# Kernel optimization log

Measured on AMD Instinct MI355X. Metric: run time of the kernel, lower is better.

The kernel has to match this reference:

```python
import jax, jax.numpy as jnp
import numpy as np

N_NODES = 100000
N_EDGES = 1600000
MAX_RADIUS = 3.0
NUM_BASIS = 3
SQRT2 = 2.0 ** 0.5
# e3nn soft_one_hot_linspace 'smooth_finite' prefactor
C_SMOOTH = 1.14136 * float(np.exp(2.0))


def _sus(x):
    # smooth unit step: exp(-1/x) for x>0 else 0 (NaN-safe for grad)
    safe = jnp.where(x > 0.0, x, 1.0)
    return jnp.where(x > 0.0, jnp.exp(-1.0 / safe), 0.0)


def radial_embed(d):
    # soft_one_hot_linspace(d, 0, max_radius, 3, basis='smooth_finite', cutoff=True) * sqrt(num_basis)
    values = jnp.linspace(0.0, MAX_RADIUS, NUM_BASIS + 2)[1:-1]  # [3]
    step = MAX_RADIUS / (NUM_BASIS + 1)
    diff = (d[:, None] - values) / step  # [E,3]
    y = C_SMOOTH * _sus(diff + 1.0) * _sus(1.0 - diff)
    return y * (NUM_BASIS ** 0.5)


def fcnet(x, w1, w2):
    # e3nn FullyConnectedNet([3,16,numel], relu): normalized weights, normalize2mom(relu)=sqrt(2)*relu
    h = SQRT2 * jax.nn.relu(x @ (w1 / w1.shape[0] ** 0.5))
    return h @ (w2 / w2.shape[0] ** 0.5)


def reference(pos, feat, edge_src, edge_dst, fc1_w1, fc1_w2, core_w1, core_w2, fc3_w1, fc3_w2, conv_w, conv_b):
    n = pos.shape[0]
    z = edge_src.shape[0] / n  # average num neighbors
    edge_vec = pos[edge_dst] - pos[edge_src]
    d = jnp.sqrt(jnp.sum(edge_vec * edge_vec, axis=1))  # edges are self-loop-free -> d > 0
    emb = radial_embed(d)  # [E,3]

    # NOTE on e3nn math: with input/mid/output parities all even and sh = 0e+1o+2e,
    # the only parity-allowed paths producing nonzero output are the 0e (scalar) paths,
    # which contract against Y_0 = 1 ('component' normalization). The 4x1e block of the
    # mid irreps is identically zero (no parity-allowed path ever populates it), so the
    # math below (scalar block only, with e3nn path weights) is exactly equivalent.
    def conv(x, w1, w2, mul_in, mul_out, path_w):
        # per-edge weights from radial MLP; keep the 0e->0e instruction block
        w = fcnet(emb, w1, w2)[:, : mul_in * mul_out].reshape(-1, mul_in, mul_out)
        msg = path_w * jnp.einsum('euw,eu->ew', w, x[edge_src])
        return jax.ops.segment_sum(msg, edge_dst, num_segments=n) / z ** 0.5

    x = conv(feat, fc1_w1, fc1_w2, 3, 4, (1.0 / 3.0) ** 0.5)  # tp1: fan_in 3*1 -> pw=1/sqrt(3)
    for i in range(3):
        x = conv(x, core_w1[i], core_w2[i], 4, 4, 0.5)  # tp2 0e path: pw=sqrt(1/4)
    x = conv(x, fc3_w1, fc3_w2, 4, 16, 0.5)  # tp3: pw=sqrt(1/4)
    # Conv1d(16, 2, 1) == pointwise linear
    return x @ conv_w.T + conv_b


def setup_inputs():
    key = jax.random.key(0)
    ks = jax.random.split(key, 12)
    pos = jax.random.uniform(ks[0], (N_NODES, 3), dtype=jnp.float32)  # unit box -> all edge lengths < max_radius
    feat = jax.random.normal(ks[1], (N_NODES, 3), dtype=jnp.float32)
    edge_src = jax.random.randint(ks[2], (N_EDGES,), 0, N_NODES, dtype=jnp.int32)
    off = jax.random.randint(ks[3], (N_EDGES,), 1, N_NODES, dtype=jnp.int32)
    edge_dst = ((edge_src + off) % N_NODES).astype(jnp.int32)  # radius_graph has no self-loops
    return {
        'pos': pos,
        'feat': feat,
        'edge_src': edge_src,
        'edge_dst': edge_dst,
        'fc1_w1': jax.random.normal(ks[4], (3, 16), jnp.float32),
        'fc1_w2': jax.random.normal(ks[5], (16, 12), jnp.float32),
        'core_w1': jax.random.normal(ks[6], (3, 3, 16), jnp.float32),
        'core_w2': jax.random.normal(ks[7], (3, 16, 48), jnp.float32),
        'fc3_w1': jax.random.normal(ks[8], (3, 16), jnp.float32),
        'fc3_w2': jax.random.normal(ks[9], (16, 64), jnp.float32),
        'conv_w': jax.random.normal(ks[10], (2, 16), jnp.float32) * 0.25,
        'conv_b': jax.random.normal(ks[11], (2,), jnp.float32) * 0.1,
    }
```

## Files before the change

### kernel.cpp

```cpp
#include <hip/hip_runtime.h>


#define BCAP 4608
#define NBMAX 400

__device__ __forceinline__ float sus_f(float x) {
    return x > 0.0f ? __expf(-1.0f / x) : 0.0f;
}

__device__ __forceinline__ float uload(const float* p) {
    return __uint_as_float(__builtin_amdgcn_readfirstlane(__float_as_uint(*p)));
}

__global__ __launch_bounds__(1024) void k_bin(
    const int* __restrict__ src, const int* __restrict__ dst,
    int* __restrict__ gcur, int* __restrict__ ptmp,
    const float* __restrict__ fc3w2, const float* __restrict__ cw,
    float* __restrict__ gbuf,
    int nedges, int nb)
{
    __shared__ int cnt[NBMAX];
    __shared__ int gb[NBMAX];
    __shared__ int lscan[NBMAX];
    __shared__ int tot;
    __shared__ unsigned short map[8192];
    __shared__ int lpk[8192];

    int t = threadIdx.x;
    if (t < NBMAX) cnt[t] = 0;
    __syncthreads();

    int base = blockIdx.x * 8192 + t * 8;
    int pk[8]; int bk[8]; short r[8];
    int ss[8], dd[8];
    if (base + 7 < nedges) {
        int4 s0 = *(const int4*)&src[base];
        int4 s1 = *(const int4*)&src[base + 4];
        int4 d0 = *(const int4*)&dst[base];
        int4 d1 = *(const int4*)&dst[base + 4];
        ss[0]=s0.x; ss[1]=s0.y; ss[2]=s0.z; ss[3]=s0.w;
        ss[4]=s1.x; ss[5]=s1.y; ss[6]=s1.z; ss[7]=s1.w;
        dd[0]=d0.x; dd[1]=d0.y; dd[2]=d0.z; dd[3]=d0.w;
        dd[4]=d1.x; dd[5]=d1.y; dd[6]=d1.z; dd[7]=d1.w;
        #pragma unroll
        for (int i = 0; i < 8; ++i) {
            int b = dd[i] >> 8;
            bk[i] = b;
            pk[i] = (ss[i] << 8) | (dd[i] & 255);
            r[i] = (short)atomicAdd(&cnt[b], 1);
        }
    } else {
        #pragma unroll
        for (int i = 0; i < 8; ++i) {
            int e = base + i;
            if (e < nedges) {
                int s = src[e], tt = dst[e];
                int b = tt >> 8;
                bk[i] = b;
                pk[i] = (s << 8) | (tt & 255);
                r[i] = (short)atomicAdd(&cnt[b], 1);
            } else bk[i] = -1;
        }
    }
    __syncthreads();

    if (t < 64) {
        int bs = t * 7;
        int c[7]; int s = 0;
        #pragma unroll
        for (int i = 0; i < 7; ++i) {
            int idx = bs + i;
            c[i] = (idx < NBMAX) ? cnt[idx] : 0;
            s += c[i];
        }
        int x = s;
        #pragma unroll
        for (int off = 1; off < 64; off <<= 1) {
            int y = __shfl_up(x, off);
            if (t >= off) x += y;
        }
        int run = x - s;
        #pragma unroll
        for (int i = 0; i < 7; ++i) {
            int idx = bs + i;
            if (idx < NBMAX) lscan[idx] = run;
            run += c[i];
        }
        if (t == 63) tot = run;
    }
    if (t < NBMAX && t < nb) {
        int c = cnt[t];
        gb[t] = c > 0 ? atomicAdd(&gcur[t], c) : 0;
    }
    __syncthreads();

    #pragma unroll
    for (int i = 0; i < 8; ++i) {
        if (bk[i] >= 0) lpk[lscan[bk[i]] + (int)r[i]] = pk[i];
    }
    if (t < NBMAX && t < nb) {
        int beg = lscan[t], end = beg + cnt[t];
        for (int j = beg; j < end; ++j) map[j] = (unsigned short)t;
    }
    __syncthreads();

    for (int j = t; j < tot; j += 1024) {
        int b = map[j];
        int p = gb[b] + (j - lscan[b]);
        if (p < BCAP)
            ptmp[b * BCAP + p] = lpk[j];
    }

    if (blockIdx.x == 0 && t < 128) {
        int idx = t;
        int k = idx >> 3, u = (idx >> 1) & 3, c = idx & 1;
        float s = 0.0f;
        #pragma unroll
        for (int w = 0; w < 16; ++w)
            s = fmaf(fc3w2[k * 64 + u * 16 + w], cw[c * 16 + w], s);
        gbuf[idx] = s;
    }
}

__global__ __launch_bounds__(1024) void k_build(
    const int* __restrict__ gcur, const int* __restrict__ ptmp,
    const float* __restrict__ pos,
    float4* __restrict__ ebuf, int2* __restrict__ offs2,
    int n, int nb)
{
    int b = blockIdx.x;
    int cnt = gcur[b]; if (cnt > BCAP) cnt = BCAP;
    int t = threadIdx.x;

    __shared__ int stage[BCAP];
    __shared__ int perm[BCAP];
    __shared__ int deg[256];
    __shared__ int loffs[256];
    __shared__ int cur[256];

    const int* tin = ptmp + b * BCAP;
    for (int j = t; j < cnt; j += 1024) stage[j] = tin[j];
    if (t < 256) deg[t] = 0;
    __syncthreads();

    for (int j = t; j < cnt; j += 1024)
        atomicAdd(&deg[stage[j] & 255], 1);
    __syncthreads();

    if (t < 64) {
        int d0 = deg[4 * t + 0], d1 = deg[4 * t + 1];
        int d2 = deg[4 * t + 2], d3 = deg[4 * t + 3];
        int s = d0 + d1 + d2 + d3;
        int x = s;
        #pragma unroll
        for (int off = 1; off < 64; off <<= 1) {
            int y = __shfl_up(x, off);
            if (t >= off) x += y;
        }
        int ex = x - s;
        int e0 = ex, e1 = ex + d0, e2 = e1 + d1, e3 = e2 + d2;
        loffs[4 * t + 0] = e0; cur[4 * t + 0] = e0;
        loffs[4 * t + 1] = e1; cur[4 * t + 1] = e1;
        loffs[4 * t + 2] = e2; cur[4 * t + 2] = e2;
        loffs[4 * t + 3] = e3; cur[4 * t + 3] = e3;
    }
    __syncthreads();

    int nid0 = b << 8;
    {
        int nn = n - nid0; if (nn > 256) nn = 256;
        if (t < nn) {
            int st = b * BCAP + loffs[t];
            offs2[nid0 + t] = make_int2(st, st + deg[t]);
        }
    }

    for (int j = t; j < cnt; j += 1024) {
        int pkd = stage[j];
        perm[atomicAdd(&cur[pkd & 255], 1)] = pkd;
    }
    __syncthreads();

    const float C = 1.14136f * 7.3890560989306495f;
    for (int j = t; j < cnt; j += 1024) {
        int pkd = perm[j];
        int s = pkd >> 8;
        int tt = nid0 | (pkd & 255);
        float dx = pos[3 * tt + 0] - pos[3 * s + 0];
        float dy = pos[3 * tt + 1] - pos[3 * s + 1];
        float dz = pos[3 * tt + 2] - pos[3 * s + 2];
        float d = sqrtf(dx * dx + dy * dy + dz * dz);
        float e0, e1, e2;
        { float f = (d - 0.75f) * (1.0f / 0.75f);
          e0 = C * sus_f(f + 1.0f) * sus_f(1.0f - f); }
        { float f = (d - 1.50f) * (1.0f / 0.75f);
          e1 = C * sus_f(f + 1.0f) * sus_f(1.0f - f); }
        { float f = (d - 2.25f) * (1.0f / 0.75f);
          e2 = C * sus_f(f + 1.0f) * sus_f(1.0f - f); }
        ebuf[(size_t)b * BCAP + j] = make_float4(__int_as_float(s), e0, e1, e2);
    }
}


__global__ __launch_bounds__(256) void k_node_l1(
    const float* __restrict__ feat, const float4* __restrict__ edata,
    const int2* __restrict__ offs2,
    const float* __restrict__ w1, const float* __restrict__ w2,
    float* __restrict__ xout, int n)
{
    __shared__ float lw[16 * 20];
    if (threadIdx.x < 192) {
        int k = threadIdx.x / 12, r = threadIdx.x % 12;
        lw[k * 20 + r] = w2[k * 12 + r];
    }
    __syncthreads();

    int g = blockIdx.x * 256 + threadIdx.x;
    int nd = g >> 2;
    if (nd >= n) return;
    int t = g & 3;

    float w1r[3][16];
    #pragma unroll
    for (int j = 0; j < 3; ++j)
        #pragma unroll
        for (int k = 0; k < 16; ++k) w1r[j][k] = uload(&w1[j * 16 + k]);

    float O[16][3];
    #pragma unroll
    for (int k = 0; k < 16; ++k)
        #pragma unroll
        for (int u = 0; u < 3; ++u) O[k][u] = 0.0f;

    int2 se = offs2[nd];
    int e = se.x + t;
    if (e < se.y) {
        float4 ed = edata[e];
        int e1 = e + 4;
        float4 edn = edata[e1 < se.y ? e1 : e];
        int s = __float_as_int(ed.x);
        float f0 = feat[3 * s + 0], f1 = feat[3 * s + 1], f2 = feat[3 * s + 2];
        while (true) {
            bool more = e1 < se.y;
            int e2 = e1 + 4;
            float4 ed2 = edata[(more && e2 < se.y) ? e2 : e];
            int sn = __float_as_int(edn.x);
            int sp = more ? sn : s;
            float f0n = feat[3 * sp + 0];
            float f1n = feat[3 * sp + 1];
            float f2n = feat[3 * sp + 2];
            #pragma unroll
            for (int k = 0; k < 16; ++k) {
                float a = fmaf(ed.y, w1r[0][k], fmaf(ed.z, w1r[1][k], ed.w * w1r[2][k]));
                float h = a > 0.0f ? a : 0.0f;
                O[k][0] = fmaf(h, f0, O[k][0]);
                O[k][1] = fmaf(h, f1, O[k][1]);
                O[k][2] = fmaf(h, f2, O[k][2]);
            }
            if (!more) break;
            ed = edn; edn = ed2;
            f0 = f0n; f1 = f1n; f2 = f2n;
            e1 = e2;
        }
    }

    float p0 = 0.f, p1 = 0.f, p2 = 0.f, p3 = 0.f;
    #pragma unroll
    for (int k = 0; k < 16; ++k)
        #pragma unroll
        for (int u = 0; u < 3; ++u) {
            const float4 q = *(const float4*)&lw[k * 20 + u * 4];
            float o = O[k][u];
            p0 = fmaf(o, q.x, p0); p1 = fmaf(o, q.y, p1);
            p2 = fmaf(o, q.z, p2); p3 = fmaf(o, q.w, p3);
        }
    p0 += __shfl_xor(p0, 1); p1 += __shfl_xor(p1, 1);
    p2 += __shfl_xor(p2, 1); p3 += __shfl_xor(p3, 1);
    p0 += __shfl_xor(p0, 2); p1 += __shfl_xor(p1, 2);
    p2 += __shfl_xor(p2, 2); p3 += __shfl_xor(p3, 2);
    if (t == 0) {
        const float S = 0.051031036307982884f;
        float4 o; o.x = p0 * S; o.y = p1 * S; o.z = p2 * S; o.w = p3 * S;
        ((float4*)xout)[nd] = o;
    }
}

__global__ __launch_bounds__(256) void k_node_core(
    const float4* __restrict__ xin, const float4* __restrict__ edata,
    const int2* __restrict__ offs2,
    const float* __restrict__ w1, const float* __restrict__ w2,
    float* __restrict__ xout, int n)
{
    __shared__ float lw[16 * 20];
    {
        int idx = threadIdx.x;
        int k = idx >> 4, r = idx & 15;
        lw[k * 20 + r] = w2[k * 48 + r];
    }
    __syncthreads();

    int g = blockIdx.x * 256 + threadIdx.x;
    int nd = g >> 2;
    if (nd >= n) return;
    int t = g & 3;

    float w1r[3][16];
    #pragma unroll
    for (int j = 0; j < 3; ++j)
        #pragma unroll
        for (int k = 0; k < 16; ++k) w1r[j][k] = uload(&w1[j * 16 + k]);

    float O[16][4];
    #pragma unroll
    for (int k = 0; k < 16; ++k)
        #pragma unroll
        for (int u = 0; u < 4; ++u) O[k][u] = 0.0f;

    int2 se = offs2[nd];
    int e = se.x + t;
    if (e < se.y) {
        float4 ed = edata[e];
        int e1 = e + 4;
        float4 edn = edata[e1 < se.y ? e1 : e];
        float4 x = xin[__float_as_int(ed.x)];
        while (true) {
            bool more = e1 < se.y;
            int e2 = e1 + 4;
            float4 ed2 = edata[(more && e2 < se.y) ? e2 : e];
            int sn = __float_as_int(edn.x);
            float4 xn = xin[more ? sn : __float_as_int(ed.x)];
            #pragma unroll
            for (int k = 0; k < 16; ++k) {
                float a = fmaf(ed.y, w1r[0][k], fmaf(ed.z, w1r[1][k], ed.w * w1r[2][k]));
                float h = a > 0.0f ? a : 0.0f;
                O[k][0] = fmaf(h, x.x, O[k][0]);
                O[k][1] = fmaf(h, x.y, O[k][1]);
                O[k][2] = fmaf(h, x.z, O[k][2]);
                O[k][3] = fmaf(h, x.w, O[k][3]);
            }
            if (!more) break;
            ed = edn; edn = ed2; x = xn; e1 = e2;
        }
    }

    float p0 = 0.f, p1 = 0.f, p2 = 0.f, p3 = 0.f;
    #pragma unroll
    for (int k = 0; k < 16; ++k)
        #pragma unroll
        for (int u = 0; u < 4; ++u) {
            const float4 q = *(const float4*)&lw[k * 20 + u * 4];
            float o = O[k][u];
            p0 = fmaf(o, q.x, p0); p1 = fmaf(o, q.y, p1);
            p2 = fmaf(o, q.z, p2); p3 = fmaf(o, q.w, p3);
        }
    p0 += __shfl_xor(p0, 1); p1 += __shfl_xor(p1, 1);
    p2 += __shfl_xor(p2, 1); p3 += __shfl_xor(p3, 1);
    p0 += __shfl_xor(p0, 2); p1 += __shfl_xor(p1, 2);
    p2 += __shfl_xor(p2, 2); p3 += __shfl_xor(p3, 2);
    if (t == 0) {
        const float S = 0.04419417382415922f;
        float4 o; o.x = p0 * S; o.y = p1 * S; o.z = p2 * S; o.w = p3 * S;
        ((float4*)xout)[nd] = o;
    }
}

__global__ __launch_bounds__(256) void k_node_fc3_final(
    const float4* __restrict__ xin, const float4* __restrict__ edata,
    const int2* __restrict__ offs2,
    const float* __restrict__ w1, const float* __restrict__ gbuf,
    const float* __restrict__ cb,
    float* __restrict__ out, int n)
{
    __shared__ float lg[128];
    if (threadIdx.x < 128) lg[threadIdx.x] = gbuf[threadIdx.x];
    __syncthreads();

    int g = blockIdx.x * 256 + threadIdx.x;
    int nd = g >> 2;
    if (nd >= n) return;
    int t = g & 3;

    float w1r[3][16];
    #pragma unroll
    for (int j = 0; j < 3; ++j)
        #pragma unroll
        for (int k = 0; k < 16; ++k) w1r[j][k] = uload(&w1[j * 16 + k]);

    float O[16][4];
    #pragma unroll
    for (int k = 0; k < 16; ++k)
        #pragma unroll
        for (int u = 0; u < 4; ++u) O[k][u] = 0.0f;

    int2 se = offs2[nd];
    int e = se.x + t;
    if (e < se.y) {
        float4 ed = edata[e];
        int e1 = e + 4;
        float4 edn = edata[e1 < se.y ? e1 : e];
        float4 x = xin[__float_as_int(ed.x)];
        while (true) {
            bool more = e1 < se.y;
            int e2 = e1 + 4;
            float4 ed2 = edata[(more && e2 < se.y) ? e2 : e];
            int sn = __float_as_int(edn.x);
            float4 xn = xin[more ? sn : __float_as_int(ed.x)];
            #pragma unroll
            for (int k = 0; k < 16; ++k) {
                float a = fmaf(ed.y, w1r[0][k], fmaf(ed.z, w1r[1][k], ed.w * w1r[2][k]));
                float h = a > 0.0f ? a : 0.0f;
                O[k][0] = fmaf(h, x.x, O[k][0]);
                O[k][1] = fmaf(h, x.y, O[k][1]);
                O[k][2] = fmaf(h, x.z, O[k][2]);
                O[k][3] = fmaf(h, x.w, O[k][3]);
            }
            if (!more) break;
            ed = edn; edn = ed2; x = xn; e1 = e2;
        }
    }

    float a0 = 0.f, a1 = 0.f;
    #pragma unroll
    for (int k = 0; k < 16; ++k)
        #pragma unroll
        for (int u = 0; u < 4; ++u) {
            float o = O[k][u];
            const float2 q = *(const float2*)&lg[(k * 4 + u) * 2];
            a0 = fmaf(o, q.x, a0);
            a1 = fmaf(o, q.y, a1);
        }
    a0 += __shfl_xor(a0, 1); a1 += __shfl_xor(a1, 1);
    a0 += __shfl_xor(a0, 2); a1 += __shfl_xor(a1, 2);
    if (t == 0) {
        const float S = 0.04419417382415922f;
        float2 o; o.x = fmaf(a0, S, cb[0]); o.y = fmaf(a1, S, cb[1]);
        ((float2*)out)[nd] = o;
    }
}


extern "C" void kernel_launch(void* const* d_in, const int* in_sizes, int n_in,
                              void* d_out, int out_size, void* d_ws, size_t ws_size,
                              hipStream_t stream) {
    const float* pos     = (const float*)d_in[0];
    const float* feat    = (const float*)d_in[1];
    const int*   esrc    = (const int*)d_in[2];
    const int*   edst    = (const int*)d_in[3];
    const float* fc1_w1  = (const float*)d_in[4];
    const float* fc1_w2  = (const float*)d_in[5];
    const float* core_w1 = (const float*)d_in[6];
    const float* core_w2 = (const float*)d_in[7];
    const float* fc3_w1  = (const float*)d_in[8];
    const float* fc3_w2  = (const float*)d_in[9];
    const float* conv_w  = (const float*)d_in[10];
    const float* conv_b  = (const float*)d_in[11];
    float* out = (float*)d_out;

    const int E = in_sizes[2];
    const int N = in_sizes[0] / 3;
    const int nb = (N + 255) >> 8;

    float4* ebuf = (float4*)d_ws;
    int* ptmp  = (int*)(ebuf + (size_t)nb * BCAP);
    float* xa  = (float*)(ptmp + (size_t)nb * BCAP);
    float* xb  = xa + (size_t)4 * N;
    int2* offs2 = (int2*)(xb + (size_t)4 * N);
    int* gcur  = (int*)(offs2 + N);
    float* gbuf = (float*)(gcur + ((nb + 3) & ~3));

    int g4 = (4 * N + 255) / 256;

    hipMemsetAsync(gcur, 0, (size_t)nb * sizeof(int), stream);
    k_bin<<<(E + 8191) / 8192, 1024, 0, stream>>>(esrc, edst, gcur, ptmp,
                                                  fc3_w2, conv_w, gbuf, E, nb);
    k_build<<<nb, 1024, 0, stream>>>(gcur, ptmp, pos, ebuf, offs2, N, nb);

    k_node_l1<<<g4, 256, 0, stream>>>(feat, ebuf, offs2, fc1_w1, fc1_w2, xa, N);
    k_node_core<<<g4, 256, 0, stream>>>((const float4*)xa, ebuf, offs2,
                                        core_w1 + 0, core_w2 + 0, xb, N);
    k_node_core<<<g4, 256, 0, stream>>>((const float4*)xb, ebuf, offs2,
                                        core_w1 + 48, core_w2 + 768, xa, N);
    k_node_core<<<g4, 256, 0, stream>>>((const float4*)xa, ebuf, offs2,
                                        core_w1 + 96, core_w2 + 1536, xb, N);
    k_node_fc3_final<<<g4, 256, 0, stream>>>((const float4*)xb, ebuf, offs2,
                                             fc3_w1, gbuf, conv_b, out, N);
}
```

Baseline: 207.3 us.

## Replace global atomic bucket scatter with per-block sorted dumps and gather in build

The binning kernel stops using global atomics to scatter edges into per-bucket slots. Each block now writes its locally sorted edge chunk contiguously, along with per-bucket counts and offsets, which also removes the memset. The build kernel prefix-scans those per-block counts and gathers each bucket's segments from every block into shared memory. The gather uses only 2*nblk threads (about 392), each doing serial strided loads, which could be slow. Edge order inside a bucket is now deterministic.

```diff
diff --git a/kernel.cpp b/kernel.cpp
--- a/kernel.cpp
+++ b/kernel.cpp
@@ -3,6 +3,7 @@
 
 #define BCAP 4608
 #define NBMAX 400
+#define EPB 8192
 
 __device__ __forceinline__ float sus_f(float x) {
     return x > 0.0f ? __expf(-1.0f / x) : 0.0f;
@@ -14,23 +15,21 @@
 
 __global__ __launch_bounds__(1024) void k_bin(
     const int* __restrict__ src, const int* __restrict__ dst,
-    int* __restrict__ gcur, int* __restrict__ ptmp,
+    int* __restrict__ ptmp, int* __restrict__ cntg, int* __restrict__ lofsg,
     const float* __restrict__ fc3w2, const float* __restrict__ cw,
     float* __restrict__ gbuf,
     int nedges, int nb)
 {
     __shared__ int cnt[NBMAX];
-    __shared__ int gb[NBMAX];
     __shared__ int lscan[NBMAX];
-    __shared__ int tot;
-    __shared__ unsigned short map[8192];
-    __shared__ int lpk[8192];
+    __shared__ int4 lpk4[EPB / 4];
+    int* lpk = (int*)lpk4;
 
     int t = threadIdx.x;
     if (t < NBMAX) cnt[t] = 0;
     __syncthreads();
 
-    int base = blockIdx.x * 8192 + t * 8;
+    int base = blockIdx.x * EPB + t * 8;
     int pk[8]; int bk[8]; short r[8];
     int ss[8], dd[8];
     if (base + 7 < nedges) {
@@ -86,29 +85,23 @@
             if (idx < NBMAX) lscan[idx] = run;
             run += c[i];
         }
-        if (t == 63) tot = run;
-    }
-    if (t < NBMAX && t < nb) {
-        int c = cnt[t];
-        gb[t] = c > 0 ? atomicAdd(&gcur[t], c) : 0;
-    }
-    __syncthreads();
+    }
+    __syncthreads();
+
+    if (t < nb) {
+        cntg[blockIdx.x * NBMAX + t] = cnt[t];
+        lofsg[blockIdx.x * NBMAX + t] = lscan[t];
+    }
 
     #pragma unroll
     for (int i = 0; i < 8; ++i) {
         if (bk[i] >= 0) lpk[lscan[bk[i]] + (int)r[i]] = pk[i];
     }
-    if (t < NBMAX && t < nb) {
-        int beg = lscan[t], end = beg + cnt[t];
-        for (int j = beg; j < end; ++j) map[j] = (unsigned short)t;
-    }
-    __syncthreads();
-
-    for (int j = t; j < tot; j += 1024) {
-        int b = map[j];
-        int p = gb[b] + (j - lscan[b]);
-        if (p < BCAP)
-            ptmp[b * BCAP + p] = lpk[j];
+    __syncthreads();
+
+    {
+        int4* o4 = (int4*)(ptmp + blockIdx.x * EPB);
+        for (int j = t; j < EPB / 4; j += 1024) o4[j] = lpk4[j];
     }
 
     if (blockIdx.x == 0 && t < 128) {
@@ -123,13 +116,12 @@
 }
 
 __global__ __launch_bounds__(1024) void k_build(
-    const int* __restrict__ gcur, const int* __restrict__ ptmp,
-    const float* __restrict__ pos,
+    const int* __restrict__ ptmp, const int* __restrict__ cntg,
+    const int* __restrict__ lofsg, const float* __restrict__ pos,
     float4* __restrict__ ebuf, int2* __restrict__ offs2,
-    int n, int nb)
+    int n, int nb, int nblk)
 {
     int b = blockIdx.x;
-    int cnt = gcur[b]; if (cnt > BCAP) cnt = BCAP;
     int t = threadIdx.x;
 
     __shared__ int stage[BCAP];
@@ -137,10 +129,53 @@
     __shared__ int deg[256];
     __shared__ int loffs[256];
     __shared__ int cur[256];
-
-    const int* tin = ptmp + b * BCAP;
-    for (int j = t; j < cnt; j += 1024) stage[j] = tin[j];
-    if (t < 256) deg[t] = 0;
+    __shared__ int scnt[256];
+    __shared__ int soff[256];
+    __shared__ int sdst[256];
+    __shared__ int total;
+
+    if (t < 256) {
+        int c = 0, o = 0;
+        if (t < nblk) { c = cntg[t * NBMAX + b]; o = lofsg[t * NBMAX + b]; }
+        scnt[t] = c; soff[t] = o;
+        deg[t] = 0;
+    }
+    __syncthreads();
+
+    if (t < 64) {
+        int c0 = scnt[4 * t + 0], c1 = scnt[4 * t + 1];
+        int c2 = scnt[4 * t + 2], c3 = scnt[4 * t + 3];
+        int s = c0 + c1 + c2 + c3;
+        int x = s;
+        #pragma unroll
+        for (int off = 1; off < 64; off <<= 1) {
+            int y = __shfl_up(x, off);
+            if (t >= off) x += y;
+        }
+        int ex = x - s;
+        sdst[4 * t + 0] = ex;
+        sdst[4 * t + 1] = ex + c0;
+        sdst[4 * t + 2] = ex + c0 + c1;
+        sdst[4 * t + 3] = ex + c0 + c1 + c2;
+        if (t == 63) total = ex + c0 + c1 + c2 + c3;
+    }
+    __syncthreads();
+
+    int cnt = total; if (cnt > BCAP) cnt = BCAP;
+
+    if (t < 2 * nblk) {
+        int i = t >> 1, half = t & 1;
+        int c = scnt[i];
+        int h0 = (c + 1) >> 1;
+        int beg = half ? h0 : 0;
+        int end = half ? c : h0;
+        const int* sp = ptmp + i * EPB + soff[i];
+        int dbase = sdst[i];
+        for (int j = beg; j < end; ++j) {
+            int d = dbase + j;
+            if (d < BCAP) stage[d] = sp[j];
+        }
+    }
     __syncthreads();
 
     for (int j = t; j < cnt; j += 1024)
@@ -459,21 +494,23 @@
     const int E = in_sizes[2];
     const int N = in_sizes[0] / 3;
     const int nb = (N + 255) >> 8;
+    const int nblk = (E + EPB - 1) / EPB;
 
     float4* ebuf = (float4*)d_ws;
     int* ptmp  = (int*)(ebuf + (size_t)nb * BCAP);
-    float* xa  = (float*)(ptmp + (size_t)nb * BCAP);
+    float* xa  = (float*)(ptmp + (size_t)nblk * EPB);
     float* xb  = xa + (size_t)4 * N;
     int2* offs2 = (int2*)(xb + (size_t)4 * N);
-    int* gcur  = (int*)(offs2 + N);
-    float* gbuf = (float*)(gcur + ((nb + 3) & ~3));
+    int* cntg  = (int*)(offs2 + N);
+    int* lofsg = cntg + (size_t)nblk * NBMAX;
+    float* gbuf = (float*)(lofsg + (size_t)nblk * NBMAX);
 
     int g4 = (4 * N + 255) / 256;
 
-    hipMemsetAsync(gcur, 0, (size_t)nb * sizeof(int), stream);
-    k_bin<<<(E + 8191) / 8192, 1024, 0, stream>>>(esrc, edst, gcur, ptmp,
-                                                  fc3_w2, conv_w, gbuf, E, nb);
-    k_build<<<nb, 1024, 0, stream>>>(gcur, ptmp, pos, ebuf, offs2, N, nb);
+    k_bin<<<nblk, 1024, 0, stream>>>(esrc, edst, ptmp, cntg, lofsg,
+                                     fc3_w2, conv_w, gbuf, E, nb);
+    k_build<<<nb, 1024, 0, stream>>>(ptmp, cntg, lofsg, pos, ebuf, offs2,
+                                     N, nb, nblk);
 
     k_node_l1<<<g4, 256, 0, stream>>>(feat, ebuf, offs2, fc1_w1, fc1_w2, xa, N);
     k_node_core<<<g4, 256, 0, stream>>>((const float4*)xa, ebuf, offs2,
```

Measured after the change: 203.1 us. 2.0% less time.
